# Kernel tuning notes

Hardware: AMD Instinct MI355X
Metric: run time of the kernel (lower is better)

The kernel has to match this reference:

```python
import jax, jax.numpy as jnp
import numpy as np

N = 50000      # nodes
E = 800000     # edges (before self-loops)
F_IN = 128
H = 4          # heads
C = 64         # per-head channels
G = 64         # graphs in batch
NEG_SLOPE = 0.2


def setup_inputs() -> dict:
    key = jax.random.key(0)
    ks = jax.random.split(key, 20)
    rn = lambda k, shape, s=0.1: (jax.random.normal(k, shape, jnp.float32) * s)
    x = jax.random.normal(ks[0], (N, F_IN), jnp.float32)
    edge_index = jax.random.randint(ks[1], (2, E), 0, N, dtype=jnp.int32)
    batch = jnp.sort(jax.random.randint(ks[2], (N,), 0, G, dtype=jnp.int32))
    return {
        "x": x, "edge_index": edge_index, "batch": batch,
        # layer 0: 128 -> (4 heads x 64), concat
        "W0": rn(ks[3], (F_IN, H * C)), "a_src0": rn(ks[4], (H, C)), "a_dst0": rn(ks[5], (H, C)), "b0": jnp.zeros((H * C,), jnp.float32),
        "W1": rn(ks[6], (H * C, H * C)), "a_src1": rn(ks[7], (H, C)), "a_dst1": rn(ks[8], (H, C)), "b1": jnp.zeros((H * C,), jnp.float32),
        "W2": rn(ks[9], (H * C, C)), "a_src2": rn(ks[10], (1, C)), "a_dst2": rn(ks[11], (1, C)), "b2": jnp.zeros((C,), jnp.float32),
        "lin_w": rn(ks[12], (C, 1)), "lin_b": jnp.zeros((1,), jnp.float32),
    }


def gat_layer(h_in, src, dst, W, a_src, a_dst, b, heads, ch, concat):
    n = h_in.shape[0]
    h = (h_in @ W).reshape(n, heads, ch)                         # [N,H,C]
    e_src = jnp.sum(h * a_src[None], axis=-1)                    # [N,H]
    e_dst = jnp.sum(h * a_dst[None], axis=-1)                    # [N,H]
    e = jax.nn.leaky_relu(e_src[src] + e_dst[dst], NEG_SLOPE)    # [E,H]
    # segment softmax over incoming edges of each destination node
    m = jax.ops.segment_max(e, dst, num_segments=n)
    m = jnp.where(jnp.isneginf(m), 0.0, m)
    ex = jnp.exp(e - m[dst])
    denom = jax.ops.segment_sum(ex, dst, num_segments=n)
    alpha = ex / (denom[dst] + 1e-16)                            # [E,H]
    out = jax.ops.segment_sum(h[src] * alpha[:, :, None], dst, num_segments=n)  # [N,H,C]
    out = out.reshape(n, heads * ch) if concat else out.mean(axis=1)
    return out + b


def reference(x, edge_index, batch, W0, a_src0, a_dst0, b0, W1, a_src1, a_dst1, b1, W2, a_src2, a_dst2, b2, lin_w, lin_b):
    n = x.shape[0]
    loops = jnp.arange(n, dtype=edge_index.dtype)
    src = jnp.concatenate([edge_index[0], loops])  # PyG add_self_loops=True
    dst = jnp.concatenate([edge_index[1], loops])
    h = jax.nn.relu(gat_layer(x, src, dst, W0, a_src0, a_dst0, b0, H, C, True))
    h = jax.nn.relu(gat_layer(h, src, dst, W1, a_src1, a_dst1, b1, H, C, True))
    h = gat_layer(h, src, dst, W2, a_src2, a_dst2, b2, 1, C, False)  # [N,64]
    # global mean pool per graph
    counts = jax.ops.segment_sum(jnp.ones((n,), h.dtype), batch, num_segments=G)
    pooled = jax.ops.segment_sum(h, batch, num_segments=G) / jnp.maximum(counts, 1.0)[:, None]
    return pooled @ lin_w + lin_b  # [G,1]
```

## Files before the change

### kernel.cpp

```cpp
#include <hip/hip_runtime.h>
#include <math.h>

typedef __bf16 bf16x8 __attribute__((ext_vector_type(8)));
typedef __bf16 bf16x4 __attribute__((ext_vector_type(4)));
typedef float f32x4 __attribute__((ext_vector_type(4)));
typedef float f32x2 __attribute__((ext_vector_type(2)));
typedef unsigned int u32x2 __attribute__((ext_vector_type(2)));
typedef unsigned int u32x4 __attribute__((ext_vector_type(4)));

#define LOG2E 1.4426950408889634f
#define BCAP 8192

static __device__ __forceinline__ float lrelu(float e) { return e > 0.0f ? e : 0.2f * e; }
static __device__ __forceinline__ float fexp2(float x) { return __builtin_amdgcn_exp2f(x); }

static __device__ __forceinline__ void dec16(u32x4 u, float* f) {
#pragma unroll
  for (int i = 0; i < 4; i++) {
    f32x2 a = __builtin_amdgcn_cvt_pk_f32_fp8(u[i], false);
    f32x2 b = __builtin_amdgcn_cvt_pk_f32_fp8(u[i], true);
    f[i * 4 + 0] = a.x;
    f[i * 4 + 1] = a.y;
    f[i * 4 + 2] = b.x;
    f[i * 4 + 3] = b.y;
  }
}

static __device__ __forceinline__ void dec8(unsigned int lo, unsigned int hi, float* f) {
  f32x2 a = __builtin_amdgcn_cvt_pk_f32_fp8(lo, false);
  f32x2 b = __builtin_amdgcn_cvt_pk_f32_fp8(lo, true);
  f32x2 c = __builtin_amdgcn_cvt_pk_f32_fp8(hi, false);
  f32x2 d = __builtin_amdgcn_cvt_pk_f32_fp8(hi, true);
  f[0] = a.x; f[1] = a.y; f[2] = b.x; f[3] = b.y;
  f[4] = c.x; f[5] = c.y; f[6] = d.x; f[7] = d.y;
}

static __device__ __forceinline__ int cmap(int p) {
  return (p & ~63) + (p & 3) * 16 + ((p & 63) >> 2);
}

__global__ void prep_kernel(const float* __restrict__ x, __bf16* __restrict__ xb, int n4,
                            const float* __restrict__ W0, __bf16* __restrict__ Bt0,
                            const float* __restrict__ W1, __bf16* __restrict__ Bt1,
                            const float* __restrict__ W2, __bf16* __restrict__ Bt2, int FIN,
                            int* __restrict__ cnt, int n) {
  int cb = (n4 + 255) / 256;
  int b = blockIdx.x;
  if (b < cb) {
    int i = b * 256 + threadIdx.x;
    if (i < n4) {
      f32x4 v = ((const f32x4*)x)[i];
      bf16x4 o = {(__bf16)v.x, (__bf16)v.y, (__bf16)v.z, (__bf16)v.w};
      ((bf16x4*)xb)[i] = o;
    }
    return;
  }
  b -= cb;
  if (b < 256) {
    for (int k = threadIdx.x; k < FIN; k += 256) Bt0[b * FIN + k] = (__bf16)W0[k * 256 + b];
    return;
  }
  b -= 256;
  if (b < 256) {
    int k = threadIdx.x;
    Bt1[b * 256 + k] = (__bf16)W1[cmap(k) * 256 + b];
    return;
  }
  b -= 256;
  if (b < 64) {
    int k = threadIdx.x;
    Bt2[b * 256 + k] = (__bf16)W2[cmap(k) * 64 + b];
    return;
  }
  b -= 64;
  int i = b * 256 + threadIdx.x;
  if (i < n) cnt[i] = 0;
}

template <int K, int NT>
__global__ __launch_bounds__(256) void gemm_part_kernel(
    const __bf16* __restrict__ A, const __bf16* __restrict__ Bt,
    const float* __restrict__ a_src, const float* __restrict__ a_dst,
    unsigned char* __restrict__ C, float* __restrict__ es, float* __restrict__ ed, int M,
    int gmx, const int* __restrict__ srcE, const int* __restrict__ dstE,
    int* __restrict__ bucket_cnt, unsigned int* __restrict__ part, int E, int EE, int n) {
  constexpr int Nc = NT * 64;
  constexpr int H = NT;
  constexpr int KS = K / 32;
  __shared__ __bf16 Bs[2][NT * 64][40];
  if ((int)blockIdx.x >= gmx) {
    int tid = threadIdx.x;
    int* hist = (int*)&Bs[0][0][0];
    int* gbase = hist + 256;
    hist[tid] = 0;
    __syncthreads();
    int ab = ((int)blockIdx.x - gmx) * 4096;
    int sv[16], dv[16];
#pragma unroll
    for (int t = 0; t < 16; t++) {
      int e = ab + t * 256 + tid;
      if (e < EE) {
        if (e < E) { sv[t] = srcE[e]; dv[t] = dstE[e]; }
        else { sv[t] = dv[t] = e - E; }
      } else { sv[t] = -1; dv[t] = 0; }
    }
    int lr[16];
#pragma unroll
    for (int t = 0; t < 16; t++)
      if (sv[t] >= 0) lr[t] = atomicAdd(&hist[dv[t] >> 8], 1);
    __syncthreads();
    int NB = (n + 255) >> 8;
    gbase[tid] = (tid < NB && hist[tid] > 0) ? atomicAdd(&bucket_cnt[tid * 16], hist[tid]) : 0;
    __syncthreads();
#pragma unroll
    for (int t = 0; t < 16; t++)
      if (sv[t] >= 0) {
        int bk = dv[t] >> 8;
        part[(size_t)bk * BCAP + gbase[bk] + lr[t]] =
            (unsigned int)sv[t] | ((unsigned int)(dv[t] & 255) << 24);
      }
    return;
  }
  int bid = blockIdx.x;
  int tid = threadIdx.x;
  int wave = tid >> 6;
  int lane = tid & 63;
  int quad = lane >> 4;
  int l16 = lane & 15;
  int rowBase = bid * 64 + wave * 16;
  f32x4 acc[NT * 4] = {};
  int arow = rowBase + l16;
  arow = (arow < M) ? arow : (M - 1);
  const __bf16* Aptr = &A[(size_t)arow * K + quad * 8];
  int sr = tid >> 2;
  int sc = (tid & 3) * 8;
  bf16x8 af[KS];
#pragma unroll
  for (int s = 0; s < KS; s++) af[s] = *(const bf16x8*)&Aptr[s * 32];
#pragma unroll
  for (int it = 0; it < NT; it++) {
    int r = it * 64 + sr;
    *(bf16x8*)&Bs[0][r][sc] = *(const bf16x8*)&Bt[(size_t)r * K + sc];
  }
  __syncthreads();
#pragma unroll
  for (int s = 0; s < KS; s++) {
    int cur = s & 1;
    if (s + 1 < KS) {
#pragma unroll
      for (int it = 0; it < NT; it++) {
        int r = it * 64 + sr;
        *(bf16x8*)&Bs[cur ^ 1][r][sc] = *(const bf16x8*)&Bt[(size_t)r * K + (s + 1) * 32 + sc];
      }
    }
#pragma unroll
    for (int ng = 0; ng < NT * 4; ng++) {
      bf16x8 b = *(const bf16x8*)&Bs[cur][ng * 16 + l16][quad * 8];
      acc[ng] = __builtin_amdgcn_mfma_f32_16x16x32_bf16(af[s], b, acc[ng], 0, 0, 0);
    }
    __syncthreads();
  }
  float asv[NT * 4], adv[NT * 4];
#pragma unroll
  for (int ng = 0; ng < NT * 4; ng++) {
    int c = (ng >> 2) * 64 + (ng & 3) * 16 + l16;
    asv[ng] = a_src[c];
    adv[ng] = a_dst[c];
  }
#pragma unroll
  for (int r = 0; r < 4; r++) {
    int row = rowBase + quad * 4 + r;
#pragma unroll
    for (int h = 0; h < H; h++) {
      float ss = 0.f, sd = 0.f;
#pragma unroll
      for (int g = 0; g < 4; g++) {
        float hv = acc[h * 4 + g][r];
        ss += hv * asv[h * 4 + g];
        sd += hv * adv[h * 4 + g];
      }
#pragma unroll
      for (int o = 1; o < 16; o <<= 1) {
        ss += __shfl_xor(ss, o);
        sd += __shfl_xor(sd, o);
      }
      if (row < M) {
        if (l16 == 0) {
          es[row * H + h] = ss * LOG2E;
          ed[row * H + h] = sd * LOG2E;
        }
        unsigned int pk = 0;
        pk = __builtin_amdgcn_cvt_pk_fp8_f32(acc[h * 4 + 0][r], acc[h * 4 + 1][r], pk, false);
        pk = __builtin_amdgcn_cvt_pk_fp8_f32(acc[h * 4 + 2][r], acc[h * 4 + 3][r], pk, true);
        *(unsigned int*)&C[(size_t)row * Nc + h * 64 + l16 * 4] = pk;
      }
    }
  }
}

__global__ __launch_bounds__(1024) void bucket_csr_kernel(
    const unsigned int* __restrict__ part, const int* __restrict__ bucket_cnt,
    int* __restrict__ offsets, int* __restrict__ src_sorted, int n, int EE) {
  __shared__ int sc[256];
  __shared__ int excl[256];
  __shared__ int run[256];
  int tid = threadIdx.x;
  int b = blockIdx.x;
  int NB = (n + 255) >> 8;
  if (tid < 256) sc[tid] = (tid < NB) ? bucket_cnt[tid * 16] : 0;
  __syncthreads();
  for (int d = 1; d < 256; d <<= 1) {
    int t = 0;
    if (tid < 256 && tid >= d) t = sc[tid - d];
    __syncthreads();
    if (tid < 256) sc[tid] += t;
    __syncthreads();
  }
  int base = (b == 0) ? 0 : sc[b - 1];
  int cb = sc[b] - base;
  const unsigned int* mypart = part + (size_t)b * BCAP;
  if (tid < 256) run[tid] = 0;
  __syncthreads();
  for (int i = tid; i < cb; i += 1024) atomicAdd(&run[mypart[i] >> 24], 1);
  __syncthreads();
  int myc = (tid < 256) ? run[tid] : 0;
  if (tid < 256) sc[tid] = myc;
  __syncthreads();
  for (int d = 1; d < 256; d <<= 1) {
    int t = 0;
    if (tid < 256 && tid >= d) t = sc[tid - d];
    __syncthreads();
    if (tid < 256) sc[tid] += t;
    __syncthreads();
  }
  if (tid < 256) {
    excl[tid] = sc[tid] - myc;
    int node = b * 256 + tid;
    if (node < n) offsets[node] = base + excl[tid];
    run[tid] = 0;
  }
  if (b == 0 && tid == 0) offsets[n] = EE;
  __syncthreads();
  for (int i = tid; i < cb; i += 1024) {
    unsigned int p = mypart[i];
    int j = p >> 24;
    int r = atomicAdd(&run[j], 1);
    src_sorted[base + excl[j] + r] = (int)(p & 0xFFFFFFu);
  }
}

template <int K, int NT>
__global__ __launch_bounds__(256) void gemm2_kernel(const __bf16* __restrict__ A,
                                                    const __bf16* __restrict__ Bt,
                                                    const float* __restrict__ a_src,
                                                    const float* __restrict__ a_dst,
                                                    unsigned char* __restrict__ C,
                                                    float* __restrict__ es,
                                                    float* __restrict__ ed, int M) {
  constexpr int Nc = NT * 64;
  constexpr int H = NT;
  constexpr int KS = K / 32;
  __shared__ __bf16 Bs[2][NT * 64][40];
  int tid = threadIdx.x;
  int wave = tid >> 6;
  int lane = tid & 63;
  int quad = lane >> 4;
  int l16 = lane & 15;
  int rowBase = blockIdx.x * 64 + wave * 16;
  f32x4 acc[NT * 4] = {};
  int arow = rowBase + l16;
  arow = (arow < M) ? arow : (M - 1);
  const __bf16* Aptr = &A[(size_t)arow * K + quad * 8];
  int sr = tid >> 2;
  int sc = (tid & 3) * 8;
  bf16x8 af[KS];
#pragma unroll
  for (int s = 0; s < KS; s++) af[s] = *(const bf16x8*)&Aptr[s * 32];
#pragma unroll
  for (int it = 0; it < NT; it++) {
    int r = it * 64 + sr;
    *(bf16x8*)&Bs[0][r][sc] = *(const bf16x8*)&Bt[(size_t)r * K + sc];
  }
  __syncthreads();
#pragma unroll
  for (int s = 0; s < KS; s++) {
    int cur = s & 1;
    if (s + 1 < KS) {
#pragma unroll
      for (int it = 0; it < NT; it++) {
        int r = it * 64 + sr;
        *(bf16x8*)&Bs[cur ^ 1][r][sc] = *(const bf16x8*)&Bt[(size_t)r * K + (s + 1) * 32 + sc];
      }
    }
#pragma unroll
    for (int ng = 0; ng < NT * 4; ng++) {
      bf16x8 b = *(const bf16x8*)&Bs[cur][ng * 16 + l16][quad * 8];
      acc[ng] = __builtin_amdgcn_mfma_f32_16x16x32_bf16(af[s], b, acc[ng], 0, 0, 0);
    }
    __syncthreads();
  }
  float asv[NT * 4], adv[NT * 4];
#pragma unroll
  for (int ng = 0; ng < NT * 4; ng++) {
    int c = (ng >> 2) * 64 + (ng & 3) * 16 + l16;
    asv[ng] = a_src[c];
    adv[ng] = a_dst[c];
  }
#pragma unroll
  for (int r = 0; r < 4; r++) {
    int row = rowBase + quad * 4 + r;
#pragma unroll
    for (int h = 0; h < H; h++) {
      float ss = 0.f, sd = 0.f;
#pragma unroll
      for (int g = 0; g < 4; g++) {
        float hv = acc[h * 4 + g][r];
        ss += hv * asv[h * 4 + g];
        sd += hv * adv[h * 4 + g];
      }
#pragma unroll
      for (int o = 1; o < 16; o <<= 1) {
        ss += __shfl_xor(ss, o);
        sd += __shfl_xor(sd, o);
      }
      if (row < M) {
        if (l16 == 0) {
          es[row * H + h] = ss * LOG2E;
          ed[row * H + h] = sd * LOG2E;
        }
        unsigned int pk = 0;
        pk = __builtin_amdgcn_cvt_pk_fp8_f32(acc[h * 4 + 0][r], acc[h * 4 + 1][r], pk, false);
        pk = __builtin_amdgcn_cvt_pk_fp8_f32(acc[h * 4 + 2][r], acc[h * 4 + 3][r], pk, true);
        *(unsigned int*)&C[(size_t)row * Nc + h * 64 + l16 * 4] = pk;
      }
    }
  }
}

__global__ void agg256_kernel(const unsigned char* __restrict__ h, const int* __restrict__ offsets,
                              const int* __restrict__ src_sorted, const float* __restrict__ es,
                              const float* __restrict__ ed, const float* __restrict__ bias,
                              __bf16* __restrict__ out, int n) {
  int node = blockIdx.x * (blockDim.x >> 6) + (threadIdx.x >> 6);
  int lane = threadIdx.x & 63;
  if (node >= n) return;
  int quad = lane >> 4;
  int l16 = lane & 15;
  int hd = l16 >> 2;
  float myEd = ed[node * 4 + hd];
  int off = offsets[node];
  int deg = offsets[node + 1] - off;
  float acc[16] = {};
  float sw = 0.f;
  int j = 0;
  int s0a = 0, s1a = 0;
  if (j + 8 <= deg) {
    s0a = src_sorted[off + j + quad];
    s1a = src_sorted[off + j + 4 + quad];
  }
  for (; j + 8 <= deg;) {
    int jn = j + 8;
    int s0 = s0a, s1 = s1a;
    if (jn + 8 <= deg) {
      s0a = src_sorted[off + jn + quad];
      s1a = src_sorted[off + jn + 4 + quad];
    }
    float e0 = es[s0 * 4 + hd];
    float e1 = es[s1 * 4 + hd];
    u32x4 u0 = *(const u32x4*)&h[(size_t)s0 * 256 + l16 * 16];
    u32x4 u1 = *(const u32x4*)&h[(size_t)s1 * 256 + l16 * 16];
    float w0 = fexp2(lrelu(e0 + myEd));
    float w1 = fexp2(lrelu(e1 + myEd));
    sw += w0 + w1;
    float f[16];
    dec16(u0, f);
#pragma unroll
    for (int k = 0; k < 16; k++) acc[k] += w0 * f[k];
    dec16(u1, f);
#pragma unroll
    for (int k = 0; k < 16; k++) acc[k] += w1 * f[k];
    j = jn;
  }
  for (; j < deg; j += 4) {
    if (quad < deg - j) {
      int s = src_sorted[off + j + quad];
      float w = fexp2(lrelu(es[s * 4 + hd] + myEd));
      sw += w;
      u32x4 u = *(const u32x4*)&h[(size_t)s * 256 + l16 * 16];
      float f[16];
      dec16(u, f);
#pragma unroll
      for (int k = 0; k < 16; k++) acc[k] += w * f[k];
    }
  }
  sw += __shfl_xor(sw, 16);
  sw += __shfl_xor(sw, 32);
#pragma unroll
  for (int k = 0; k < 16; k++) {
    acc[k] += __shfl_xor(acc[k], 16);
    acc[k] += __shfl_xor(acc[k], 32);
  }
  float invS = 1.0f / (sw + 1e-16f);
  if (quad == 0) {
    bf16x8 o0, o1;
#pragma unroll
    for (int k = 0; k < 16; k++) {
      int c = hd * 64 + (k & 3) * 16 + (l16 & 3) * 4 + (k >> 2);
      float v = fmaxf(acc[k] * invS + bias[c], 0.f);
      if (k < 8) o0[k] = (__bf16)v; else o1[k - 8] = (__bf16)v;
    }
    *(bf16x8*)&out[(size_t)node * 256 + l16 * 16] = o0;
    *(bf16x8*)&out[(size_t)node * 256 + l16 * 16 + 8] = o1;
  }
}

__global__ void agg64_kernel(const unsigned char* __restrict__ h, const int* __restrict__ offsets,
                             const int* __restrict__ src_sorted, const float* __restrict__ es,
                             const float* __restrict__ ed, const float* __restrict__ bias,
                             const float* __restrict__ lin_w, float* __restrict__ pnode, int n) {
  int node = blockIdx.x * (blockDim.x >> 6) + (threadIdx.x >> 6);
  int lane = threadIdx.x & 63;
  if (node >= n) return;
  int grp = lane >> 3;
  int l8 = lane & 7;
  float myEd = ed[node];
  int off = offsets[node];
  int deg = offsets[node + 1] - off;
  float acc[8] = {};
  float sw = 0.f;
  int j = 0;
  for (; j + 8 <= deg; j += 8) {
    int s = src_sorted[off + j + grp];
    float w = fexp2(lrelu(es[s] + myEd));
    sw += w;
    u32x2 u = *(const u32x2*)&h[(size_t)s * 64 + l8 * 8];
    float f[8];
    dec8(u.x, u.y, f);
#pragma unroll
    for (int k = 0; k < 8; k++) acc[k] += w * f[k];
  }
  if (j < deg && grp < deg - j) {
    int s = src_sorted[off + j + grp];
    float w = fexp2(lrelu(es[s] + myEd));
    sw += w;
    u32x2 u = *(const u32x2*)&h[(size_t)s * 64 + l8 * 8];
    float f[8];
    dec8(u.x, u.y, f);
#pragma unroll
    for (int k = 0; k < 8; k++) acc[k] += w * f[k];
  }
#pragma unroll
  for (int o = 8; o < 64; o <<= 1) {
    sw += __shfl_xor(sw, o);
#pragma unroll
    for (int k = 0; k < 8; k++) acc[k] += __shfl_xor(acc[k], o);
  }
  float invS = 1.0f / (sw + 1e-16f);
  float p = 0.f;
#pragma unroll
  for (int k = 0; k < 8; k++) {
    int c = (k & 3) * 16 + l8 * 2 + (k >> 2);
    p += (acc[k] * invS + bias[c]) * lin_w[c];
  }
#pragma unroll
  for (int o = 1; o < 8; o <<= 1) p += __shfl_xor(p, o);
  if (lane == 0) pnode[node] = p;
}

static __device__ __forceinline__ int lowerb(const int* __restrict__ a, int n, int key) {
  int lo = 0, hi = n;
  while (lo < hi) {
    int mid = (lo + hi) >> 1;
    if (a[mid] < key) lo = mid + 1; else hi = mid;
  }
  return lo;
}

__global__ void poolfinal_kernel(const float* __restrict__ pnode, const int* __restrict__ batch,
                                 const float* __restrict__ lin_b, float* __restrict__ out, int n) {
  __shared__ float ws[4];
  int g = blockIdx.x;
  int start = lowerb(batch, n, g);
  int end = lowerb(batch, n, g + 1);
  float acc = 0.f;
  for (int i = start + threadIdx.x; i < end; i += 256) acc += pnode[i];
  for (int o = 32; o > 0; o >>= 1) acc += __shfl_down(acc, o);
  if ((threadIdx.x & 63) == 0) ws[threadIdx.x >> 6] = acc;
  __syncthreads();
  if (threadIdx.x == 0) {
    float total = ws[0] + ws[1] + ws[2] + ws[3];
    out[g] = total / fmaxf((float)(end - start), 1.0f) + lin_b[0];
  }
}

extern "C" void kernel_launch(void* const* d_in, const int* in_sizes, int n_in, void* d_out,
                              int out_size, void* d_ws, size_t ws_size, hipStream_t stream) {
  const float* x = (const float*)d_in[0];
  const int* edge_index = (const int*)d_in[1];
  const int* batch = (const int*)d_in[2];
  const float* W0 = (const float*)d_in[3];
  const float* a_src0 = (const float*)d_in[4];
  const float* a_dst0 = (const float*)d_in[5];
  const float* b0 = (const float*)d_in[6];
  const float* W1 = (const float*)d_in[7];
  const float* a_src1 = (const float*)d_in[8];
  const float* a_dst1 = (const float*)d_in[9];
  const float* b1 = (const float*)d_in[10];
  const float* W2 = (const float*)d_in[11];
  const float* a_src2 = (const float*)d_in[12];
  const float* a_dst2 = (const float*)d_in[13];
  const float* b2 = (const float*)d_in[14];
  const float* lin_w = (const float*)d_in[15];
  const float* lin_b = (const float*)d_in[16];
  float* out = (float*)d_out;

  const int N = in_sizes[2];
  const int E = in_sizes[1] / 2;
  const int EE = E + N;
  const int G = 64;
  const int FIN = in_sizes[0] / N;

  const int* srcArr = edge_index;
  const int* dstArr = edge_index + E;

  size_t off = 0;
  auto alloc = [&](size_t bytes) -> void* {
    off = (off + 255) & ~(size_t)255;
    void* p = (char*)d_ws + off;
    off += bytes;
    return p;
  };
  __bf16* xb = (__bf16*)alloc((size_t)N * FIN * 2);
  unsigned char* hA = (unsigned char*)alloc((size_t)N * 256);
  __bf16* hB = (__bf16*)alloc((size_t)N * 256 * 2);
  unsigned char* h2 = (unsigned char*)alloc((size_t)N * 64);
  float* pnode = (float*)alloc((size_t)N * 4);
  __bf16* Bt0 = (__bf16*)alloc((size_t)256 * FIN * 2);
  __bf16* Bt1 = (__bf16*)alloc((size_t)256 * 256 * 2);
  __bf16* Bt2 = (__bf16*)alloc((size_t)64 * 256 * 2);
  float* es = (float*)alloc((size_t)N * 4 * 4);
  float* ed = (float*)alloc((size_t)N * 4 * 4);
  int* offsets = (int*)alloc((size_t)(N + 1) * 4);
  int* src_sorted = (int*)alloc((size_t)EE * 4);
  int* bucket_cnt = (int*)alloc((size_t)4096 * 4);
  (void)ws_size;

  int NB = (N + 255) >> 8;

  unsigned int* part = (unsigned int*)hB;

  int n4 = N * FIN / 4;
  int cb = (n4 + 255) / 256;
  int nwb = (N + 3) / 4;
  int gmx = (N + 63) / 64;
  int nA = (EE + 4095) / 4096;

  prep_kernel<<<cb + 576 + 16, 256, 0, stream>>>(x, xb, n4, W0, Bt0, W1, Bt1, W2, Bt2, FIN,
                                                 bucket_cnt, 4096);

  gemm_part_kernel<128, 4><<<gmx + nA, 256, 0, stream>>>(
      xb, Bt0, a_src0, a_dst0, hA, es, ed, N, gmx, srcArr, dstArr, bucket_cnt, part, E, EE, N);

  bucket_csr_kernel<<<NB, 1024, 0, stream>>>(part, bucket_cnt, offsets, src_sorted, N, EE);

  agg256_kernel<<<nwb, 256, 0, stream>>>(hA, offsets, src_sorted, es, ed, b0, hB, N);

  gemm2_kernel<256, 4><<<gmx, 256, 0, stream>>>(hB, Bt1, a_src1, a_dst1, hA, es, ed, N);
  agg256_kernel<<<nwb, 256, 0, stream>>>(hA, offsets, src_sorted, es, ed, b1, hB, N);

  gemm2_kernel<256, 1><<<gmx, 256, 0, stream>>>(hB, Bt2, a_src2, a_dst2, h2, es, ed, N);
  agg64_kernel<<<nwb, 256, 0, stream>>>(h2, offsets, src_sorted, es, ed, b2, lin_w, pnode, N);

  poolfinal_kernel<<<G, 256, 0, stream>>>(pnode, batch, lin_b, out, N);
}
```

Before: 286.1 us.

## Fuse GAT aggregation into the next layer's GEMM and convert x in-kernel

Merges each agg256 pass with the following GEMM: each block aggregates 64 destination nodes into an LDS bf16 tile, then runs the MFMA GEMM straight from LDS, so the bf16 hidden matrix never makes a round trip through global memory. The first GEMM now reads fp32 x and converts to bf16 in registers, which drops the separate conversion pass in prep. Two launches disappear, at the cost of per-node serial aggregation inside each wave (16 nodes per wave), a 32KB LDS A tile that may lower occupancy, and a single-buffered B tile. Per-layer es/ed buffers are split so one layer's outputs can be written while the previous layer's are still being read.

```diff
diff --git a/kernel.cpp b/kernel.cpp
--- a/kernel.cpp
+++ b/kernel.cpp
@@ -39,23 +39,11 @@
   return (p & ~63) + (p & 3) * 16 + ((p & 63) >> 2);
 }
 
-__global__ void prep_kernel(const float* __restrict__ x, __bf16* __restrict__ xb, int n4,
-                            const float* __restrict__ W0, __bf16* __restrict__ Bt0,
+__global__ void prep_kernel(const float* __restrict__ W0, __bf16* __restrict__ Bt0,
                             const float* __restrict__ W1, __bf16* __restrict__ Bt1,
                             const float* __restrict__ W2, __bf16* __restrict__ Bt2, int FIN,
                             int* __restrict__ cnt, int n) {
-  int cb = (n4 + 255) / 256;
   int b = blockIdx.x;
-  if (b < cb) {
-    int i = b * 256 + threadIdx.x;
-    if (i < n4) {
-      f32x4 v = ((const f32x4*)x)[i];
-      bf16x4 o = {(__bf16)v.x, (__bf16)v.y, (__bf16)v.z, (__bf16)v.w};
-      ((bf16x4*)xb)[i] = o;
-    }
-    return;
-  }
-  b -= cb;
   if (b < 256) {
     for (int k = threadIdx.x; k < FIN; k += 256) Bt0[b * FIN + k] = (__bf16)W0[k * 256 + b];
     return;
@@ -79,7 +67,7 @@
 
 template <int K, int NT>
 __global__ __launch_bounds__(256) void gemm_part_kernel(
-    const __bf16* __restrict__ A, const __bf16* __restrict__ Bt,
+    const float* __restrict__ A, const __bf16* __restrict__ Bt,
     const float* __restrict__ a_src, const float* __restrict__ a_dst,
     unsigned char* __restrict__ C, float* __restrict__ es, float* __restrict__ ed, int M,
     int gmx, const int* __restrict__ srcE, const int* __restrict__ dstE,
@@ -131,12 +119,19 @@
   f32x4 acc[NT * 4] = {};
   int arow = rowBase + l16;
   arow = (arow < M) ? arow : (M - 1);
-  const __bf16* Aptr = &A[(size_t)arow * K + quad * 8];
+  const float* Aptr = &A[(size_t)arow * K + quad * 8];
   int sr = tid >> 2;
   int sc = (tid & 3) * 8;
   bf16x8 af[KS];
 #pragma unroll
-  for (int s = 0; s < KS; s++) af[s] = *(const bf16x8*)&Aptr[s * 32];
+  for (int s = 0; s < KS; s++) {
+    f32x4 lo = *(const f32x4*)&Aptr[s * 32];
+    f32x4 hi = *(const f32x4*)&Aptr[s * 32 + 4];
+    bf16x8 t;
+    t[0] = (__bf16)lo.x; t[1] = (__bf16)lo.y; t[2] = (__bf16)lo.z; t[3] = (__bf16)lo.w;
+    t[4] = (__bf16)hi.x; t[5] = (__bf16)hi.y; t[6] = (__bf16)hi.z; t[7] = (__bf16)hi.w;
+    af[s] = t;
+  }
 #pragma unroll
   for (int it = 0; it < NT; it++) {
     int r = it * 64 + sr;
@@ -249,53 +244,118 @@
   }
 }
 
-template <int K, int NT>
-__global__ __launch_bounds__(256) void gemm2_kernel(const __bf16* __restrict__ A,
-                                                    const __bf16* __restrict__ Bt,
-                                                    const float* __restrict__ a_src,
-                                                    const float* __restrict__ a_dst,
-                                                    unsigned char* __restrict__ C,
-                                                    float* __restrict__ es,
-                                                    float* __restrict__ ed, int M) {
+template <int NT>
+__global__ __launch_bounds__(256) void agg_gemm_kernel(
+    const unsigned char* __restrict__ hin, const int* __restrict__ offsets,
+    const int* __restrict__ src_sorted, const float* __restrict__ esL,
+    const float* __restrict__ edL, const float* __restrict__ biasL,
+    const __bf16* __restrict__ Bt, const float* __restrict__ a_srcN,
+    const float* __restrict__ a_dstN, unsigned char* __restrict__ C,
+    float* __restrict__ esN, float* __restrict__ edN, int M) {
   constexpr int Nc = NT * 64;
   constexpr int H = NT;
-  constexpr int KS = K / 32;
-  __shared__ __bf16 Bs[2][NT * 64][40];
+  __shared__ __bf16 Atile[64][256];
+  __shared__ __bf16 Bs[NT * 64][40];
   int tid = threadIdx.x;
   int wave = tid >> 6;
   int lane = tid & 63;
   int quad = lane >> 4;
   int l16 = lane & 15;
-  int rowBase = blockIdx.x * 64 + wave * 16;
-  f32x4 acc[NT * 4] = {};
-  int arow = rowBase + l16;
-  arow = (arow < M) ? arow : (M - 1);
-  const __bf16* Aptr = &A[(size_t)arow * K + quad * 8];
+  int hd = l16 >> 2;
+  for (int i = 0; i < 16; i++) {
+    int lr = wave * 16 + i;
+    int node = blockIdx.x * 64 + lr;
+    float accv[16] = {};
+    float sw = 0.f;
+    float myEd = 0.f;
+    int off = 0, deg = 0;
+    if (node < M) {
+      myEd = edL[node * 4 + hd];
+      off = offsets[node];
+      deg = offsets[node + 1] - off;
+    }
+    int j = 0;
+    int s0a = 0, s1a = 0;
+    if (j + 8 <= deg) {
+      s0a = src_sorted[off + quad];
+      s1a = src_sorted[off + 4 + quad];
+    }
+    for (; j + 8 <= deg;) {
+      int jn = j + 8;
+      int s0 = s0a, s1 = s1a;
+      if (jn + 8 <= deg) {
+        s0a = src_sorted[off + jn + quad];
+        s1a = src_sorted[off + jn + 4 + quad];
+      }
+      float e0 = esL[s0 * 4 + hd];
+      float e1 = esL[s1 * 4 + hd];
+      u32x4 u0 = *(const u32x4*)&hin[(size_t)s0 * 256 + l16 * 16];
+      u32x4 u1 = *(const u32x4*)&hin[(size_t)s1 * 256 + l16 * 16];
+      float w0 = fexp2(lrelu(e0 + myEd));
+      float w1 = fexp2(lrelu(e1 + myEd));
+      sw += w0 + w1;
+      float f[16];
+      dec16(u0, f);
+#pragma unroll
+      for (int k = 0; k < 16; k++) accv[k] += w0 * f[k];
+      dec16(u1, f);
+#pragma unroll
+      for (int k = 0; k < 16; k++) accv[k] += w1 * f[k];
+      j = jn;
+    }
+    for (; j < deg; j += 4) {
+      if (quad < deg - j) {
+        int s = src_sorted[off + j + quad];
+        float w = fexp2(lrelu(esL[s * 4 + hd] + myEd));
+        sw += w;
+        u32x4 u = *(const u32x4*)&hin[(size_t)s * 256 + l16 * 16];
+        float f[16];
+        dec16(u, f);
+#pragma unroll
+        for (int k = 0; k < 16; k++) accv[k] += w * f[k];
+      }
+    }
+    sw += __shfl_xor(sw, 16);
+    sw += __shfl_xor(sw, 32);
+#pragma unroll
+    for (int k = 0; k < 16; k++) {
+      accv[k] += __shfl_xor(accv[k], 16);
+      accv[k] += __shfl_xor(accv[k], 32);
+    }
+    if (quad == 0) {
+      float invS = 1.0f / (sw + 1e-16f);
+      bf16x8 o0, o1;
+#pragma unroll
+      for (int k = 0; k < 16; k++) {
+        int c = hd * 64 + (k & 3) * 16 + (l16 & 3) * 4 + (k >> 2);
+        float v = (node < M) ? fmaxf(accv[k] * invS + biasL[c], 0.f) : 0.f;
+        if (k < 8) o0[k] = (__bf16)v; else o1[k - 8] = (__bf16)v;
+      }
+      *(bf16x8*)&Atile[lr][l16 * 16] = o0;
+      *(bf16x8*)&Atile[lr][l16 * 16 + 8] = o1;
+    }
+  }
+  __syncthreads();
   int sr = tid >> 2;
   int sc = (tid & 3) * 8;
-  bf16x8 af[KS];
-#pragma unroll
-  for (int s = 0; s < KS; s++) af[s] = *(const bf16x8*)&Aptr[s * 32];
-#pragma unroll
-  for (int it = 0; it < NT; it++) {
-    int r = it * 64 + sr;
-    *(bf16x8*)&Bs[0][r][sc] = *(const bf16x8*)&Bt[(size_t)r * K + sc];
-  }
-  __syncthreads();
-#pragma unroll
-  for (int s = 0; s < KS; s++) {
-    int cur = s & 1;
-    if (s + 1 < KS) {
-#pragma unroll
-      for (int it = 0; it < NT; it++) {
-        int r = it * 64 + sr;
-        *(bf16x8*)&Bs[cur ^ 1][r][sc] = *(const bf16x8*)&Bt[(size_t)r * K + (s + 1) * 32 + sc];
-      }
-    }
+  int rowBase = blockIdx.x * 64 + wave * 16;
+  int arow_l = wave * 16 + l16;
+  bf16x8 af[8];
+#pragma unroll
+  for (int s = 0; s < 8; s++) af[s] = *(const bf16x8*)&Atile[arow_l][quad * 8 + s * 32];
+  f32x4 acc[NT * 4] = {};
+#pragma unroll
+  for (int kb = 0; kb < 8; kb++) {
+#pragma unroll
+    for (int it = 0; it < NT; it++) {
+      int r = it * 64 + sr;
+      *(bf16x8*)&Bs[r][sc] = *(const bf16x8*)&Bt[(size_t)r * 256 + kb * 32 + sc];
+    }
+    __syncthreads();
 #pragma unroll
     for (int ng = 0; ng < NT * 4; ng++) {
-      bf16x8 b = *(const bf16x8*)&Bs[cur][ng * 16 + l16][quad * 8];
-      acc[ng] = __builtin_amdgcn_mfma_f32_16x16x32_bf16(af[s], b, acc[ng], 0, 0, 0);
+      bf16x8 b = *(const bf16x8*)&Bs[ng * 16 + l16][quad * 8];
+      acc[ng] = __builtin_amdgcn_mfma_f32_16x16x32_bf16(af[kb], b, acc[ng], 0, 0, 0);
     }
     __syncthreads();
   }
@@ -303,8 +363,8 @@
 #pragma unroll
   for (int ng = 0; ng < NT * 4; ng++) {
     int c = (ng >> 2) * 64 + (ng & 3) * 16 + l16;
-    asv[ng] = a_src[c];
-    adv[ng] = a_dst[c];
+    asv[ng] = a_srcN[c];
+    adv[ng] = a_dstN[c];
   }
 #pragma unroll
   for (int r = 0; r < 4; r++) {
@@ -325,8 +385,8 @@
       }
       if (row < M) {
         if (l16 == 0) {
-          es[row * H + h] = ss * LOG2E;
-          ed[row * H + h] = sd * LOG2E;
+          esN[row * H + h] = ss * LOG2E;
+          edN[row * H + h] = sd * LOG2E;
         }
         unsigned int pk = 0;
         pk = __builtin_amdgcn_cvt_pk_fp8_f32(acc[h * 4 + 0][r], acc[h * 4 + 1][r], pk, false);
@@ -334,83 +394,6 @@
         *(unsigned int*)&C[(size_t)row * Nc + h * 64 + l16 * 4] = pk;
       }
     }
-  }
-}
-
-__global__ void agg256_kernel(const unsigned char* __restrict__ h, const int* __restrict__ offsets,
-                              const int* __restrict__ src_sorted, const float* __restrict__ es,
-                              const float* __restrict__ ed, const float* __restrict__ bias,
-                              __bf16* __restrict__ out, int n) {
-  int node = blockIdx.x * (blockDim.x >> 6) + (threadIdx.x >> 6);
-  int lane = threadIdx.x & 63;
-  if (node >= n) return;
-  int quad = lane >> 4;
-  int l16 = lane & 15;
-  int hd = l16 >> 2;
-  float myEd = ed[node * 4 + hd];
-  int off = offsets[node];
-  int deg = offsets[node + 1] - off;
-  float acc[16] = {};
-  float sw = 0.f;
-  int j = 0;
-  int s0a = 0, s1a = 0;
-  if (j + 8 <= deg) {
-    s0a = src_sorted[off + j + quad];
-    s1a = src_sorted[off + j + 4 + quad];
-  }
-  for (; j + 8 <= deg;) {
-    int jn = j + 8;
-    int s0 = s0a, s1 = s1a;
-    if (jn + 8 <= deg) {
-      s0a = src_sorted[off + jn + quad];
-      s1a = src_sorted[off + jn + 4 + quad];
-    }
-    float e0 = es[s0 * 4 + hd];
-    float e1 = es[s1 * 4 + hd];
-    u32x4 u0 = *(const u32x4*)&h[(size_t)s0 * 256 + l16 * 16];
-    u32x4 u1 = *(const u32x4*)&h[(size_t)s1 * 256 + l16 * 16];
-    float w0 = fexp2(lrelu(e0 + myEd));
-    float w1 = fexp2(lrelu(e1 + myEd));
-    sw += w0 + w1;
-    float f[16];
-    dec16(u0, f);
-#pragma unroll
-    for (int k = 0; k < 16; k++) acc[k] += w0 * f[k];
-    dec16(u1, f);
-#pragma unroll
-    for (int k = 0; k < 16; k++) acc[k] += w1 * f[k];
-    j = jn;
-  }
-  for (; j < deg; j += 4) {
-    if (quad < deg - j) {
-      int s = src_sorted[off + j + quad];
-      float w = fexp2(lrelu(es[s * 4 + hd] + myEd));
-      sw += w;
-      u32x4 u = *(const u32x4*)&h[(size_t)s * 256 + l16 * 16];
-      float f[16];
-      dec16(u, f);
-#pragma unroll
-      for (int k = 0; k < 16; k++) acc[k] += w * f[k];
-    }
-  }
-  sw += __shfl_xor(sw, 16);
-  sw += __shfl_xor(sw, 32);
-#pragma unroll
-  for (int k = 0; k < 16; k++) {
-    acc[k] += __shfl_xor(acc[k], 16);
-    acc[k] += __shfl_xor(acc[k], 32);
-  }
-  float invS = 1.0f / (sw + 1e-16f);
-  if (quad == 0) {
-    bf16x8 o0, o1;
-#pragma unroll
-    for (int k = 0; k < 16; k++) {
-      int c = hd * 64 + (k & 3) * 16 + (l16 & 3) * 4 + (k >> 2);
-      float v = fmaxf(acc[k] * invS + bias[c], 0.f);
-      if (k < 8) o0[k] = (__bf16)v; else o1[k - 8] = (__bf16)v;
-    }
-    *(bf16x8*)&out[(size_t)node * 256 + l16 * 16] = o0;
-    *(bf16x8*)&out[(size_t)node * 256 + l16 * 16 + 8] = o1;
   }
 }
 
@@ -530,16 +513,19 @@
     off += bytes;
     return p;
   };
-  __bf16* xb = (__bf16*)alloc((size_t)N * FIN * 2);
   unsigned char* hA = (unsigned char*)alloc((size_t)N * 256);
-  __bf16* hB = (__bf16*)alloc((size_t)N * 256 * 2);
+  unsigned char* hC = (unsigned char*)alloc((size_t)N * 256);
   unsigned char* h2 = (unsigned char*)alloc((size_t)N * 64);
   float* pnode = (float*)alloc((size_t)N * 4);
   __bf16* Bt0 = (__bf16*)alloc((size_t)256 * FIN * 2);
   __bf16* Bt1 = (__bf16*)alloc((size_t)256 * 256 * 2);
   __bf16* Bt2 = (__bf16*)alloc((size_t)64 * 256 * 2);
-  float* es = (float*)alloc((size_t)N * 4 * 4);
-  float* ed = (float*)alloc((size_t)N * 4 * 4);
+  float* es0 = (float*)alloc((size_t)N * 4 * 4);
+  float* ed0 = (float*)alloc((size_t)N * 4 * 4);
+  float* es1 = (float*)alloc((size_t)N * 4 * 4);
+  float* ed1 = (float*)alloc((size_t)N * 4 * 4);
+  float* es2 = (float*)alloc((size_t)N * 4);
+  float* ed2 = (float*)alloc((size_t)N * 4);
   int* offsets = (int*)alloc((size_t)(N + 1) * 4);
   int* src_sorted = (int*)alloc((size_t)EE * 4);
   int* bucket_cnt = (int*)alloc((size_t)4096 * 4);
@@ -547,29 +533,26 @@
 
   int NB = (N + 255) >> 8;
 
-  unsigned int* part = (unsigned int*)hB;
-
-  int n4 = N * FIN / 4;
-  int cb = (n4 + 255) / 256;
+  unsigned int* part = (unsigned int*)hC;
+
   int nwb = (N + 3) / 4;
   int gmx = (N + 63) / 64;
   int nA = (EE + 4095) / 4096;
 
-  prep_kernel<<<cb + 576 + 16, 256, 0, stream>>>(x, xb, n4, W0, Bt0, W1, Bt1, W2, Bt2, FIN,
-                                                 bucket_cnt, 4096);
+  prep_kernel<<<576 + 16, 256, 0, stream>>>(W0, Bt0, W1, Bt1, W2, Bt2, FIN, bucket_cnt, 4096);
 
   gemm_part_kernel<128, 4><<<gmx + nA, 256, 0, stream>>>(
-      xb, Bt0, a_src0, a_dst0, hA, es, ed, N, gmx, srcArr, dstArr, bucket_cnt, part, E, EE, N);
+      x, Bt0, a_src0, a_dst0, hA, es0, ed0, N, gmx, srcArr, dstArr, bucket_cnt, part, E, EE, N);
 
   bucket_csr_kernel<<<NB, 1024, 0, stream>>>(part, bucket_cnt, offsets, src_sorted, N, EE);
 
-  agg256_kernel<<<nwb, 256, 0, stream>>>(hA, offsets, src_sorted, es, ed, b0, hB, N);
-
-  gemm2_kernel<256, 4><<<gmx, 256, 0, stream>>>(hB, Bt1, a_src1, a_dst1, hA, es, ed, N);
-  agg256_kernel<<<nwb, 256, 0, stream>>>(hA, offsets, src_sorted, es, ed, b1, hB, N);
-
-  gemm2_kernel<256, 1><<<gmx, 256, 0, stream>>>(hB, Bt2, a_src2, a_dst2, h2, es, ed, N);
-  agg64_kernel<<<nwb, 256, 0, stream>>>(h2, offsets, src_sorted, es, ed, b2, lin_w, pnode, N);
+  agg_gemm_kernel<4><<<gmx, 256, 0, stream>>>(hA, offsets, src_sorted, es0, ed0, b0, Bt1,
+                                              a_src1, a_dst1, hC, es1, ed1, N);
+
+  agg_gemm_kernel<1><<<gmx, 256, 0, stream>>>(hC, offsets, src_sorted, es1, ed1, b1, Bt2,
+                                              a_src2, a_dst2, h2, es2, ed2, N);
+
+  agg64_kernel<<<nwb, 256, 0, stream>>>(h2, offsets, src_sorted, es2, ed2, b2, lin_w, pnode, N);
 
   poolfinal_kernel<<<G, 256, 0, stream>>>(pnode, batch, lin_b, out, N);
 }
```

Result: slower. 466.5 us (+63.0%).
